# Kernel optimization log

Measured on AMD Instinct MI355X. Metric: run time of the kernel, lower is better.

The kernel has to match this reference:

```python
import jax, jax.numpy as jnp
import numpy as np

N_BINS = 256
HOP = 80


def _gru(xs, Wih, Whh, bih, bhh, reverse=False):
    """Single-layer unidirectional GRU, PyTorch gate layout (r, z, n).
    xs: (T, B, I); Wih: (3H, I); Whh: (3H, H). Returns (T, B, H)."""
    H = Whh.shape[1]
    gi = jnp.einsum('tbi,gi->tbg', xs, Wih) + bih  # precompute input projections

    def step(h, gi_t):
        gh = h @ Whh.T + bhh
        ir, iz, inn = jnp.split(gi_t, 3, axis=-1)
        hr, hz, hn = jnp.split(gh, 3, axis=-1)
        r = jax.nn.sigmoid(ir + hr)
        z = jax.nn.sigmoid(iz + hz)
        n = jnp.tanh(inn + r * hn)
        h_new = (1.0 - z) * n + z * h
        return h_new, h_new

    h0 = jnp.zeros((xs.shape[1], H), xs.dtype)
    _, ys = jax.lax.scan(step, h0, gi, reverse=reverse)
    return ys


def _quantize(w):
    # continuous [-1, 1] -> bin index in [0, N_BINS-1]
    return jnp.clip(jnp.floor((w + 1.0) * (N_BINS / 2)), 0, N_BINS - 1).astype(jnp.int32)


def _forward(x, y, p):
    # --- encode: 2-layer bidirectional GRU over mel frames ---
    c = x
    for l in ('m0', 'm1'):
        f = _gru(c, p[l + 'f_Wih'], p[l + 'f_Whh'], p[l + 'f_bih'], p[l + 'f_bhh'])
        bwd = _gru(c, p[l + 'b_Wih'], p[l + 'b_Whh'], p[l + 'b_bih'], p[l + 'b_bhh'], reverse=True)
        c = jnp.concatenate([f, bwd], axis=-1)  # (t_m, b, 2*dim_enc)
    # nearest-neighbor upsample in time (matches F.interpolate default 'nearest')
    c = jnp.repeat(c, HOP, axis=0)  # (t_w, b, 2*dim_enc)

    # --- teacher forcing: shift waveform right, vectorize via embedding ---
    b = x.shape[1]
    w = jnp.concatenate([jnp.zeros((1, b), y.dtype), y[:-1]], axis=0)
    e = p['E'][_quantize(w)]  # (t_w, b, dim_vec)

    # --- wav GRU + projection + GELU ---
    o = _gru(jnp.concatenate([e, c], axis=-1), p['w_Wih'], p['w_Whh'], p['w_bih'], p['w_bhh'])
    o = jax.nn.gelu(o @ p['Wp'].T + p['bp'], approximate=False)  # (t_w, b, dim_proj)

    # --- categorical neg log prob over quantized targets ---
    logits = o @ p['Wd'].T + p['bd']  # (t_w, b, N_BINS)
    logp = jax.nn.log_softmax(logits, axis=-1)
    tgt = _quantize(y)
    nll = -jnp.mean(jnp.take_along_axis(logp, tgt[..., None], axis=-1))
    return nll


def setup_inputs() -> dict:
    key = jax.random.key(0)
    ks = iter(jax.random.split(key, 64))

    def rn(shape, s=0.08):
        return jax.random.normal(next(ks), shape, jnp.float32) * s

    t_m, b, dm = 32, 4, 80
    de, dv, dd, dp = 128, 256, 896, 512
    d = {}
    d['x'] = jax.random.normal(next(ks), (t_m, b, dm), jnp.float32)
    d['y'] = jax.random.uniform(next(ks), (t_m * HOP, b), jnp.float32, minval=-1.0, maxval=1.0)
    for name, i in [('m0f', dm), ('m0b', dm), ('m1f', 2 * de), ('m1b', 2 * de)]:
        d[name + '_Wih'] = rn((3 * de, i))
        d[name + '_Whh'] = rn((3 * de, de))
        d[name + '_bih'] = rn((3 * de,))
        d[name + '_bhh'] = rn((3 * de,))
    d['w_Wih'] = rn((3 * dd, 2 * de + dv))
    d['w_Whh'] = rn((3 * dd, dd))
    d['w_bih'] = rn((3 * dd,))
    d['w_bhh'] = rn((3 * dd,))
    d['Wp'] = rn((dp, dd))
    d['bp'] = rn((dp,))
    d['E'] = rn((N_BINS, dv))
    d['Wd'] = rn((N_BINS, dp))
    d['bd'] = rn((N_BINS,))
    return d


def reference(x, y, m0f_Wih, m0f_Whh, m0f_bih, m0f_bhh, m0b_Wih, m0b_Whh, m0b_bih, m0b_bhh,
              m1f_Wih, m1f_Whh, m1f_bih, m1f_bhh, m1b_Wih, m1b_Whh, m1b_bih, m1b_bhh,
              w_Wih, w_Whh, w_bih, w_bhh, Wp, bp, E, Wd, bd):
    p = dict(m0f_Wih=m0f_Wih, m0f_Whh=m0f_Whh, m0f_bih=m0f_bih, m0f_bhh=m0f_bhh,
             m0b_Wih=m0b_Wih, m0b_Whh=m0b_Whh, m0b_bih=m0b_bih, m0b_bhh=m0b_bhh,
             m1f_Wih=m1f_Wih, m1f_Whh=m1f_Whh, m1f_bih=m1f_bih, m1f_bhh=m1f_bhh,
             m1b_Wih=m1b_Wih, m1b_Whh=m1b_Whh, m1b_bih=m1b_bih, m1b_bhh=m1b_bhh,
             w_Wih=w_Wih, w_Whh=w_Whh, w_bih=w_bih, w_bhh=w_bhh,
             Wp=Wp, bp=bp, E=E, Wd=Wd, bd=bd)
    return _forward(x, y, p)
```

## Files before the change

### kernel.cpp

```cpp
#include <hip/hip_runtime.h>
#include <stdint.h>
#include <math.h>

typedef __attribute__((ext_vector_type(8))) short bf16x8;
typedef __attribute__((ext_vector_type(4))) float f32x4;
typedef __attribute__((ext_vector_type(4))) unsigned int u32x4;

#define BATCH 4
#define T_M 32
#define DE 128
#define T_W 2560
#define NWG 56

__device__ __forceinline__ float b2f(unsigned short h) {
  return __uint_as_float(((unsigned int)h) << 16);
}
__device__ __forceinline__ unsigned short f2b(float f) {
  unsigned int u = __float_as_uint(f);
  u = u + 0x7fffu + ((u >> 16) & 1u);
  return (unsigned short)(u >> 16);
}
__device__ __forceinline__ float blo(unsigned int u){ return __uint_as_float(u << 16); }
__device__ __forceinline__ float bhi(unsigned int u){ return __uint_as_float(u & 0xffff0000u); }
__device__ __forceinline__ float sigm(float x){
  return __builtin_amdgcn_rcpf(1.f + __expf(-x));
}
__device__ __forceinline__ float tanh_fast(float x){
  float x2 = fminf(fmaxf(x + x, -30.f), 30.f);
  return 1.f - 2.f * __builtin_amdgcn_rcpf(__expf(x2) + 1.f);
}
__device__ __forceinline__ float gelu_exact(float x){ return 0.5f * x * (1.f + erff(x * 0.70710678118654752f)); }

__global__ __launch_bounds__(256) void k_cast(const float* __restrict__ src,
                                              unsigned short* __restrict__ dst, int n)
{
  int i = blockIdx.x * 256 + threadIdx.x;
  if (i < n) dst[i] = f2b(src[i]);
}

__global__ __launch_bounds__(256) void k_prep_whh(const float* __restrict__ whh,
                                                  unsigned short* __restrict__ out)
{
  int idx = blockIdx.x * 256 + threadIdx.x;
  if (idx >= 224 * 28 * 512) return;
  int j    = idx & 7;
  int r16  = (idx >> 3) & 15;
  int quad = (idx >> 7) & 3;
  int kc   = (idx >> 9) % 28;
  int G    = (idx >> 9) / 28;
  unsigned short val = 0;
  if (r16 < 12) {
    int row = (r16 >> 2) * 896 + G * 4 + (r16 & 3);
    int col = kc * 32 + quad * 8 + j;
    val = f2b(whh[(size_t)row * 896 + col]);
  }
  out[idx] = val;
}

__global__ __launch_bounds__(384) void k_gi_enc(
    const float* __restrict__ in, const float* __restrict__ Wih,
    const float* __restrict__ bih, float* __restrict__ out, int K)
{
  __shared__ float in_s[256];
  int tb = blockIdx.x;
  for (int i = threadIdx.x; i < K; i += 384) in_s[i] = in[tb * K + i];
  __syncthreads();
  int row = threadIdx.x;
  float acc = bih[row];
  const float* wr = Wih + row * K;
  for (int k = 0; k < K; ++k) acc += in_s[k] * wr[k];
  out[tb * 384 + row] = acc;
}

__global__ __launch_bounds__(512) void k_scan_enc(
    const float* __restrict__ gi_f, const float* __restrict__ gi_b,
    const float* __restrict__ whh_f, const float* __restrict__ bhh_f,
    const float* __restrict__ whh_b, const float* __restrict__ bhh_b,
    float* __restrict__ c_out)
{
  const int dir = blockIdx.x, tid = threadIdx.x;
  const float* gi  = dir ? gi_b  : gi_f;
  const float* whh = dir ? whh_b : whh_f;
  const float* bhh = dir ? bhh_b : bhh_f;
  __shared__ unsigned short h_s[BATCH][DE + 8];
  __shared__ float gh_s[384][4];
  __shared__ float bhh_s[384];
  for (int i = tid; i < 384; i += 512) bhh_s[i] = bhh[i];
  for (int i = tid; i < BATCH * (DE + 8); i += 512) ((unsigned short*)h_s)[i] = 0;
  __syncthreads();
  for (int s = 0; s < T_M; ++s) {
    int t = dir ? (T_M - 1 - s) : s;
    #pragma unroll
    for (int k3 = 0; k3 < 3; ++k3) {
      int d = tid + 512 * k3;
      int row = d >> 2, b = d & 3;
      const float* wr = whh + row * DE;
      float acc = 0.f;
      for (int j = 0; j < DE; j += 8) {
        float4 w0 = *(const float4*)(wr + j);
        float4 w1 = *(const float4*)(wr + j + 4);
        uint4  hv = *(const uint4*)&h_s[b][j];
        acc += w0.x * blo(hv.x) + w0.y * bhi(hv.x) + w0.z * blo(hv.y) + w0.w * bhi(hv.y);
        acc += w1.x * blo(hv.z) + w1.y * bhi(hv.z) + w1.z * blo(hv.w) + w1.w * bhi(hv.w);
      }
      gh_s[row][b] = acc + bhh_s[row];
    }
    __syncthreads();
    {
      int u = tid >> 2, b = tid & 3;
      const float* git = gi + (t * BATCH + b) * 384;
      float r = sigm(git[u] + gh_s[u][b]);
      float z = sigm(git[DE + u] + gh_s[DE + u][b]);
      float n = tanh_fast(git[2 * DE + u] + r * gh_s[2 * DE + u][b]);
      float hold = b2f(h_s[b][u]);
      float hnew = (1.f - z) * n + z * hold;
      c_out[(t * BATCH + b) * 256 + dir * DE + u] = hnew;
      h_s[b][u] = f2b(hnew);
    }
    __syncthreads();
  }
}

__global__ __launch_bounds__(256) void k_mgemm(
    const unsigned short* __restrict__ A, const unsigned short* __restrict__ B,
    const float* __restrict__ bias, void* __restrict__ C,
    int M, int N, int K, int act, int c_bf16, int swz, int afuse,
    const unsigned short* __restrict__ Eb, const unsigned short* __restrict__ c1b,
    const float* __restrict__ yw)
{
  __shared__ unsigned short As[128][40];
  __shared__ unsigned short Bs[128][40];
  const int tid = threadIdx.x;
  const int m0 = blockIdx.x * 128, n0 = blockIdx.y * 128;
  const int lane = tid & 63, wave = tid >> 6;
  const int wy = wave >> 1, wx = wave & 1;
  const int row16 = lane & 15, quad = lane >> 4;
  const int sr = tid >> 1, sc = (tid & 1) * 16;
  const unsigned short* arow0 = nullptr;
  const unsigned short* arow1 = nullptr;
  if (afuse) {
    int row = m0 + sr, tt = row >> 2, b = row & 3;
    float w = (tt == 0) ? 0.f : yw[(tt - 1) * 4 + b];
    int q = (int)floorf((w + 1.f) * 128.f);
    q = q < 0 ? 0 : (q > 255 ? 255 : q);
    arow0 = Eb + q * 256;
    arow1 = c1b + ((tt / 80) * 4 + b) * 256;
  }
  f32x4 acc[4][4] = {};
  for (int kt = 0; kt < K; kt += 32) {
    uint4 av, av2;
    if (afuse) {
      int kk = kt + sc;
      const unsigned short* src = (kk < 256) ? (arow0 + kk) : (arow1 + kk - 256);
      av  = *(const uint4*)src;
      av2 = *(const uint4*)(src + 8);
    } else {
      av  = *(const uint4*)(A + (size_t)(m0 + sr) * K + kt + sc);
      av2 = *(const uint4*)(A + (size_t)(m0 + sr) * K + kt + sc + 8);
    }
    uint4 bv  = *(const uint4*)(B + (size_t)(n0 + sr) * K + kt + sc);
    uint4 bv2 = *(const uint4*)(B + (size_t)(n0 + sr) * K + kt + sc + 8);
    __syncthreads();
    *(uint4*)&As[sr][sc] = av; *(uint4*)&As[sr][sc + 8] = av2;
    *(uint4*)&Bs[sr][sc] = bv; *(uint4*)&Bs[sr][sc + 8] = bv2;
    __syncthreads();
    bf16x8 af[4], bf[4];
    #pragma unroll
    for (int i = 0; i < 4; ++i) af[i] = *(const bf16x8*)&As[wy * 64 + i * 16 + row16][quad * 8];
    #pragma unroll
    for (int j = 0; j < 4; ++j) bf[j] = *(const bf16x8*)&Bs[wx * 64 + j * 16 + row16][quad * 8];
    #pragma unroll
    for (int i = 0; i < 4; ++i)
      #pragma unroll
      for (int j = 0; j < 4; ++j)
        acc[i][j] = __builtin_amdgcn_mfma_f32_16x16x32_bf16(af[i], bf[j], acc[i][j], 0, 0, 0);
  }
  #pragma unroll
  for (int i = 0; i < 4; ++i) {
    #pragma unroll
    for (int j = 0; j < 4; ++j) {
      int col = n0 + wx * 64 + j * 16 + row16;
      float bs = bias[col];
      #pragma unroll
      for (int r = 0; r < 4; ++r) {
        int row = m0 + wy * 64 + i * 16 + quad * 4 + r;
        float v = acc[i][j][r] + bs;
        if (act) v = gelu_exact(v);
        if (swz) {
          int t = row >> 2, b = row & 3;
          int g = col / 896, rem = col - g * 896;
          int G = rem >> 2, u = rem & 3;
          ((unsigned short*)C)[(size_t)(t * 224 + G) * 48 + g * 16 + b * 4 + u] = f2b(v);
        } else if (c_bf16) {
          ((unsigned short*)C)[(size_t)row * N + col] = f2b(v);
        } else {
          ((float*)C)[(size_t)row * N + col] = v;
        }
      }
    }
  }
}

__global__ __launch_bounds__(256, 1) void k_wav_rnn(
    const unsigned short* __restrict__ whh_p,
    const float* __restrict__ bhh,
    const unsigned short* __restrict__ gp_,
    unsigned int* __restrict__ hslots,
    unsigned int* __restrict__ O32)
{
  const int wg = blockIdx.x, tid = threadIdx.x;
  const int lane = tid & 63, wave = tid >> 6;
  const int G = wg * 4 + wave;

  __shared__ unsigned short h_lds[2][4][912];
  __shared__ float phh[4][3][4][4];

  const int r16 = lane & 15, quad = lane >> 4, bb = lane & 3;
  const int fu = (lane >> 2) & 3, fb = lane & 3;

  bf16x8 wf[28];
  {
    const bf16x8* W8 = (const bf16x8*)whh_p + (size_t)G * 28 * 64;
    #pragma unroll
    for (int kc = 0; kc < 28; ++kc)
      wf[kc] = W8[(kc * 4 + quad) * 16 + r16];
  }

  const float br_ = bhh[G * 4 + fu];
  const float bz_ = bhh[896 + G * 4 + fu];
  const float bn_ = bhh[1792 + G * 4 + fu];
  float hprev = 0.f;
  const unsigned short* gl0 = gp_ + (size_t)G * 48 + fb * 4 + fu;
  unsigned short cr = gl0[0], cz = gl0[16], cn = gl0[32];

  const int p0 = tid, p1 = tid + 256, p2 = tid + 512;
  const int p3 = (tid < 128) ? tid + 768 : tid;
  const int pb0 = p0 / 224, pG0 = p0 - pb0 * 224;
  const int pb1 = p1 / 224, pG1 = p1 - pb1 * 224;
  const int pb2 = p2 / 224, pG2 = p2 - pb2 * 224;
  const int pb3 = p3 / 224, pG3 = p3 - pb3 * 224;

  const unsigned long long base0 = (unsigned long long)hslots;
  const unsigned long long base1 = base0 + 14336ull;

  for (int t = 0; t < T_W; ++t) {
    const unsigned long long hb = (t & 1) ? base1 : base0;
    unsigned long long a0 = hb + ((unsigned long long)p0 << 4);
    unsigned long long a1 = hb + ((unsigned long long)p1 << 4);
    unsigned long long a2 = hb + ((unsigned long long)p2 << 4);
    unsigned long long a3 = hb + ((unsigned long long)p3 << 4);
    u32x4 s0, s1, s2, s3;
    const unsigned int tg = (unsigned int)t;
    for (;;) {
      asm volatile(
        "global_load_dwordx4 %0, %4, off sc0 sc1\n"
        "global_load_dwordx4 %1, %5, off sc0 sc1\n"
        "global_load_dwordx4 %2, %6, off sc0 sc1\n"
        "global_load_dwordx4 %3, %7, off sc0 sc1\n"
        "s_waitcnt vmcnt(0)"
        : "=&v"(s0), "=&v"(s1), "=&v"(s2), "=&v"(s3)
        : "v"(a0), "v"(a1), "v"(a2), "v"(a3)
        : "memory");
      unsigned int bad = (s0.z ^ tg) | (s1.z ^ tg) | (s2.z ^ tg) | (s3.z ^ tg);
      if (!__any(bad != 0)) break;
      __builtin_amdgcn_s_sleep(1);
    }

    int tn = (t + 1 < T_W) ? (t + 1) : t;
    const unsigned short* gp = gp_ + (size_t)tn * 10752 + G * 48 + fb * 4 + fu;
    unsigned short nr_ = gp[0], nz_ = gp[16], nn_ = gp[32];

    *(uint2*)&h_lds[t & 1][pb0][pG0 * 4] = make_uint2(s0.x, s0.y);
    *(uint2*)&h_lds[t & 1][pb1][pG1 * 4] = make_uint2(s1.x, s1.y);
    *(uint2*)&h_lds[t & 1][pb2][pG2 * 4] = make_uint2(s2.x, s2.y);
    *(uint2*)&h_lds[t & 1][pb3][pG3 * 4] = make_uint2(s3.x, s3.y);
    __syncthreads();

    f32x4 ac0 = {}, ac1 = {}, ac2 = {}, ac3 = {};
    #pragma unroll
    for (int kc = 0; kc < 28; kc += 4) {
      bf16x8 h0 = *(const bf16x8*)&h_lds[t & 1][bb][(kc + 0) * 32 + quad * 8];
      bf16x8 h1 = *(const bf16x8*)&h_lds[t & 1][bb][(kc + 1) * 32 + quad * 8];
      bf16x8 h2 = *(const bf16x8*)&h_lds[t & 1][bb][(kc + 2) * 32 + quad * 8];
      bf16x8 h3 = *(const bf16x8*)&h_lds[t & 1][bb][(kc + 3) * 32 + quad * 8];
      ac0 = __builtin_amdgcn_mfma_f32_16x16x32_bf16(wf[kc + 0], h0, ac0, 0, 0, 0);
      ac1 = __builtin_amdgcn_mfma_f32_16x16x32_bf16(wf[kc + 1], h1, ac1, 0, 0, 0);
      ac2 = __builtin_amdgcn_mfma_f32_16x16x32_bf16(wf[kc + 2], h2, ac2, 0, 0, 0);
      ac3 = __builtin_amdgcn_mfma_f32_16x16x32_bf16(wf[kc + 3], h3, ac3, 0, 0, 0);
    }
    f32x4 ac;
    ac[0] = ac0[0] + ac1[0] + ac2[0] + ac3[0];
    ac[1] = ac0[1] + ac1[1] + ac2[1] + ac3[1];
    ac[2] = ac0[2] + ac1[2] + ac2[2] + ac3[2];
    ac[3] = ac0[3] + ac1[3] + ac2[3] + ac3[3];

    if (r16 < 4 && quad < 3)
      *(f32x4*)&phh[wave][quad][r16][0] = ac;
    asm volatile("s_waitcnt lgkmcnt(0)" ::: "memory");

    float pr = phh[wave][0][fb][fu];
    float pz = phh[wave][1][fb][fu];
    float pn = phh[wave][2][fb][fu];
    float r = sigm(b2f(cr) + br_ + pr);
    float z = sigm(b2f(cz) + bz_ + pz);
    float n = tanh_fast(b2f(cn) + bn_ + r * pn);
    float h = (1.f - z) * n + z * hprev;
    hprev = h;
    unsigned int hu = f2b(h);
    cr = nr_; cz = nz_; cn = nn_;

    int b = lane & 3;
    unsigned int u0v = (unsigned int)__shfl((int)hu, 0 + b);
    unsigned int u1v = (unsigned int)__shfl((int)hu, 4 + b);
    unsigned int u2v = (unsigned int)__shfl((int)hu, 8 + b);
    unsigned int u3v = (unsigned int)__shfl((int)hu, 12 + b);
    if (lane < 4) {
      u32x4 pkt;
      pkt.x = (u0v & 0xffffu) | (u1v << 16);
      pkt.y = (u2v & 0xffffu) | (u3v << 16);
      pkt.z = (unsigned int)(t + 1);
      pkt.w = 0u;
      unsigned long long sa = (((t + 1) & 1) ? base1 : base0)
                            + (unsigned long long)((b * 224 + G) << 4);
      asm volatile("global_store_dwordx4 %0, %1, off sc0 sc1"
                   :: "v"(sa), "v"(pkt) : "memory");
      *(uint2*)(O32 + (size_t)(t * 4 + b) * 448 + G * 2) = make_uint2(pkt.x, pkt.y);
    }
  }
}

__global__ __launch_bounds__(256) void k_nll(
    const float* __restrict__ logits, const float* __restrict__ y,
    float* __restrict__ acc)
{
  int wid = threadIdx.x >> 6, lane = threadIdx.x & 63;
  int row = blockIdx.x * 4 + wid;
  const float* lr = logits + (size_t)row * 256;
  float v0 = lr[lane], v1 = lr[lane + 64], v2 = lr[lane + 128], v3 = lr[lane + 192];
  float mx = fmaxf(fmaxf(v0, v1), fmaxf(v2, v3));
  for (int off = 32; off > 0; off >>= 1) mx = fmaxf(mx, __shfl_xor(mx, off));
  float se = __expf(v0 - mx) + __expf(v1 - mx) + __expf(v2 - mx) + __expf(v3 - mx);
  for (int off = 32; off > 0; off >>= 1) se += __shfl_xor(se, off);
  if (lane == 0) {
    float w = y[row];
    int q = (int)floorf((w + 1.f) * 128.f);
    q = q < 0 ? 0 : (q > 255 ? 255 : q);
    float contrib = (logf(se) + mx) - lr[q];
    atomicAdd(acc, contrib);
  }
}

__global__ void k_final(const float* __restrict__ acc, float* __restrict__ out) {
  out[0] = acc[0] * (1.f / 10240.f);
}

extern "C" void kernel_launch(void* const* d_in, const int* in_sizes, int n_in,
                              void* d_out, int out_size, void* d_ws, size_t ws_size,
                              hipStream_t stream)
{
  const float* x       = (const float*)d_in[0];
  const float* y       = (const float*)d_in[1];
  const float* m0f_Wih = (const float*)d_in[2];
  const float* m0f_Whh = (const float*)d_in[3];
  const float* m0f_bih = (const float*)d_in[4];
  const float* m0f_bhh = (const float*)d_in[5];
  const float* m0b_Wih = (const float*)d_in[6];
  const float* m0b_Whh = (const float*)d_in[7];
  const float* m0b_bih = (const float*)d_in[8];
  const float* m0b_bhh = (const float*)d_in[9];
  const float* m1f_Wih = (const float*)d_in[10];
  const float* m1f_Whh = (const float*)d_in[11];
  const float* m1f_bih = (const float*)d_in[12];
  const float* m1f_bhh = (const float*)d_in[13];
  const float* m1b_Wih = (const float*)d_in[14];
  const float* m1b_Whh = (const float*)d_in[15];
  const float* m1b_bih = (const float*)d_in[16];
  const float* m1b_bhh = (const float*)d_in[17];
  const float* w_Wih   = (const float*)d_in[18];
  const float* w_Whh   = (const float*)d_in[19];
  const float* w_bih   = (const float*)d_in[20];
  const float* w_bhh   = (const float*)d_in[21];
  const float* Wp      = (const float*)d_in[22];
  const float* bp      = (const float*)d_in[23];
  const float* E       = (const float*)d_in[24];
  const float* Wd      = (const float*)d_in[25];
  const float* bd      = (const float*)d_in[26];

  char* ws = (char*)d_ws;
  size_t off = 0;
  auto alloc = [&](size_t bytes) -> void* {
    void* p = ws + off;
    off += (bytes + 255) & ~(size_t)255;
    return p;
  };
  float*        nacc   = (float*)alloc(64);
  unsigned int* hslots = (unsigned int*)alloc(2 * 896 * 16);
  size_t misc_bytes = off;

  float* c0   = (float*)alloc((size_t)32 * 4 * 256 * 4);
  float* c1   = (float*)alloc((size_t)32 * 4 * 256 * 4);
  float* gi0f = (float*)alloc((size_t)32 * 4 * 384 * 4);
  float* gi0b = (float*)alloc((size_t)32 * 4 * 384 * 4);
  float* gi1f = (float*)alloc((size_t)32 * 4 * 384 * 4);
  float* gi1b = (float*)alloc((size_t)32 * 4 * 384 * 4);
  unsigned short* Eb    = (unsigned short*)alloc((size_t)256 * 256 * 2);
  unsigned short* c1b   = (unsigned short*)alloc((size_t)32 * 4 * 256 * 2);
  unsigned short* gpack = (unsigned short*)alloc((size_t)2560 * 224 * 48 * 2);
  unsigned int*   O32   = (unsigned int*)alloc((size_t)10240 * 448 * 4);
  unsigned short* O2    = (unsigned short*)alloc((size_t)10240 * 512 * 2);
  float*          LG    = (float*)alloc((size_t)10240 * 256 * 4);
  unsigned short* Wih_b = (unsigned short*)alloc((size_t)2688 * 512 * 2);
  unsigned short* Whh_p = (unsigned short*)alloc((size_t)224 * 28 * 512 * 2);
  unsigned short* Wp_b  = (unsigned short*)alloc((size_t)512 * 896 * 2);
  unsigned short* Wd_b  = (unsigned short*)alloc((size_t)256 * 512 * 2);

  hipMemsetAsync(d_ws, 0, misc_bytes, stream);

  k_cast<<<(2688 * 512 + 255) / 256, 256, 0, stream>>>(w_Wih, Wih_b, 2688 * 512);
  k_cast<<<(512 * 896 + 255) / 256, 256, 0, stream>>>(Wp, Wp_b, 512 * 896);
  k_cast<<<(256 * 512 + 255) / 256, 256, 0, stream>>>(Wd, Wd_b, 256 * 512);
  k_cast<<<(256 * 256 + 255) / 256, 256, 0, stream>>>(E, Eb, 256 * 256);
  k_prep_whh<<<(224 * 28 * 512 + 255) / 256, 256, 0, stream>>>(w_Whh, Whh_p);

  k_gi_enc<<<128, 384, 0, stream>>>(x, m0f_Wih, m0f_bih, gi0f, 80);
  k_gi_enc<<<128, 384, 0, stream>>>(x, m0b_Wih, m0b_bih, gi0b, 80);
  k_scan_enc<<<2, 512, 0, stream>>>(gi0f, gi0b, m0f_Whh, m0f_bhh, m0b_Whh, m0b_bhh, c0);
  k_gi_enc<<<128, 384, 0, stream>>>(c0, m1f_Wih, m1f_bih, gi1f, 256);
  k_gi_enc<<<128, 384, 0, stream>>>(c0, m1b_Wih, m1b_bih, gi1b, 256);
  k_scan_enc<<<2, 512, 0, stream>>>(gi1f, gi1b, m1f_Whh, m1f_bhh, m1b_Whh, m1b_bhh, c1);
  k_cast<<<(32 * 4 * 256 + 255) / 256, 256, 0, stream>>>(c1, c1b, 32 * 4 * 256);

  k_mgemm<<<dim3(80, 21), 256, 0, stream>>>(nullptr, Wih_b, w_bih, (void*)gpack,
                                            10240, 2688, 512, 0, 1, 1, 1, Eb, c1b, y);

  k_wav_rnn<<<NWG, 256, 0, stream>>>(Whh_p, w_bhh, gpack, hslots, O32);

  k_mgemm<<<dim3(80, 4), 256, 0, stream>>>((const unsigned short*)O32, Wp_b, bp,
                                           (void*)O2, 10240, 512, 896, 1, 1, 0, 0,
                                           nullptr, nullptr, nullptr);
  k_mgemm<<<dim3(80, 2), 256, 0, stream>>>(O2, Wd_b, bd, (void*)LG,
                                           10240, 256, 512, 0, 0, 0, 0,
                                           nullptr, nullptr, nullptr);
  k_nll<<<2560, 256, 0, stream>>>(LG, y, nacc);
  k_final<<<1, 1, 0, stream>>>(nacc, (float*)d_out);
}
```

Before: 6.020 ms.

## Merge prep casts, fuse c1 cast into scan, drop spin sleep, tree-reduce NLL

Merges the four weight-cast kernels and the Whh pack kernel into one launch, and has the second encoder scan write the bf16 copy of its output so the separate cast launch goes away. The gi_enc dot product is vectorised with float4 loads. The s_sleep in the wav-RNN spin-wait is removed to cut polling latency on the serial recurrence, at the cost of heavier memory polling. The NLL atomic accumulation is replaced by per-block partials plus a 256-thread reduction, which also makes the sum order deterministic.

```diff
diff --git a/kernel.cpp b/kernel.cpp
--- a/kernel.cpp
+++ b/kernel.cpp
@@ -31,17 +31,24 @@
 }
 __device__ __forceinline__ float gelu_exact(float x){ return 0.5f * x * (1.f + erff(x * 0.70710678118654752f)); }
 
-__global__ __launch_bounds__(256) void k_cast(const float* __restrict__ src,
-                                              unsigned short* __restrict__ dst, int n)
-{
-  int i = blockIdx.x * 256 + threadIdx.x;
-  if (i < n) dst[i] = f2b(src[i]);
-}
-
-__global__ __launch_bounds__(256) void k_prep_whh(const float* __restrict__ whh,
-                                                  unsigned short* __restrict__ out)
+__global__ __launch_bounds__(256) void k_prep(
+    const float* __restrict__ wih, const float* __restrict__ wp,
+    const float* __restrict__ wd, const float* __restrict__ e,
+    const float* __restrict__ whh,
+    unsigned short* __restrict__ wih_b, unsigned short* __restrict__ wp_b,
+    unsigned short* __restrict__ wd_b, unsigned short* __restrict__ eb,
+    unsigned short* __restrict__ whh_p)
 {
   int idx = blockIdx.x * 256 + threadIdx.x;
+  const int N0 = 2688 * 512, N1 = 512 * 896, N2 = 256 * 512, N3 = 256 * 256;
+  if (idx < N0) { wih_b[idx] = f2b(wih[idx]); return; }
+  idx -= N0;
+  if (idx < N1) { wp_b[idx] = f2b(wp[idx]); return; }
+  idx -= N1;
+  if (idx < N2) { wd_b[idx] = f2b(wd[idx]); return; }
+  idx -= N2;
+  if (idx < N3) { eb[idx] = f2b(e[idx]); return; }
+  idx -= N3;
   if (idx >= 224 * 28 * 512) return;
   int j    = idx & 7;
   int r16  = (idx >> 3) & 15;
@@ -54,7 +61,7 @@
     int col = kc * 32 + quad * 8 + j;
     val = f2b(whh[(size_t)row * 896 + col]);
   }
-  out[idx] = val;
+  whh_p[idx] = val;
 }
 
 __global__ __launch_bounds__(384) void k_gi_enc(
@@ -68,7 +75,11 @@
   int row = threadIdx.x;
   float acc = bih[row];
   const float* wr = Wih + row * K;
-  for (int k = 0; k < K; ++k) acc += in_s[k] * wr[k];
+  for (int k = 0; k < K; k += 4) {
+    float4 w = *(const float4*)(wr + k);
+    float4 v = *(const float4*)(in_s + k);
+    acc += w.x * v.x + w.y * v.y + w.z * v.z + w.w * v.w;
+  }
   out[tb * 384 + row] = acc;
 }
 
@@ -76,7 +87,7 @@
     const float* __restrict__ gi_f, const float* __restrict__ gi_b,
     const float* __restrict__ whh_f, const float* __restrict__ bhh_f,
     const float* __restrict__ whh_b, const float* __restrict__ bhh_b,
-    float* __restrict__ c_out)
+    float* __restrict__ c_out, unsigned short* __restrict__ cb)
 {
   const int dir = blockIdx.x, tid = threadIdx.x;
   const float* gi  = dir ? gi_b  : gi_f;
@@ -114,7 +125,9 @@
       float n = tanh_fast(git[2 * DE + u] + r * gh_s[2 * DE + u][b]);
       float hold = b2f(h_s[b][u]);
       float hnew = (1.f - z) * n + z * hold;
-      c_out[(t * BATCH + b) * 256 + dir * DE + u] = hnew;
+      int oi = (t * BATCH + b) * 256 + dir * DE + u;
+      c_out[oi] = hnew;
+      if (cb) cb[oi] = f2b(hnew);
       h_s[b][u] = f2b(hnew);
     }
     __syncthreads();
@@ -263,7 +276,6 @@
         : "memory");
       unsigned int bad = (s0.z ^ tg) | (s1.z ^ tg) | (s2.z ^ tg) | (s3.z ^ tg);
       if (!__any(bad != 0)) break;
-      __builtin_amdgcn_s_sleep(1);
     }
 
     int tn = (t + 1 < T_W) ? (t + 1) : t;
@@ -331,8 +343,9 @@
 
 __global__ __launch_bounds__(256) void k_nll(
     const float* __restrict__ logits, const float* __restrict__ y,
-    float* __restrict__ acc)
-{
+    float* __restrict__ partials)
+{
+  __shared__ float ps[4];
   int wid = threadIdx.x >> 6, lane = threadIdx.x & 63;
   int row = blockIdx.x * 4 + wid;
   const float* lr = logits + (size_t)row * 256;
@@ -345,13 +358,23 @@
     float w = y[row];
     int q = (int)floorf((w + 1.f) * 128.f);
     q = q < 0 ? 0 : (q > 255 ? 255 : q);
-    float contrib = (logf(se) + mx) - lr[q];
-    atomicAdd(acc, contrib);
-  }
-}
-
-__global__ void k_final(const float* __restrict__ acc, float* __restrict__ out) {
-  out[0] = acc[0] * (1.f / 10240.f);
+    ps[wid] = (logf(se) + mx) - lr[q];
+  }
+  __syncthreads();
+  if (threadIdx.x == 0) partials[blockIdx.x] = ps[0] + ps[1] + ps[2] + ps[3];
+}
+
+__global__ __launch_bounds__(256) void k_final(const float* __restrict__ partials,
+                                               float* __restrict__ out)
+{
+  __shared__ float s[4];
+  int tid = threadIdx.x;
+  float a = 0.f;
+  for (int i = tid; i < 2560; i += 256) a += partials[i];
+  for (int off = 32; off > 0; off >>= 1) a += __shfl_xor(a, off);
+  if ((tid & 63) == 0) s[tid >> 6] = a;
+  __syncthreads();
+  if (tid == 0) out[0] = (s[0] + s[1] + s[2] + s[3]) * (1.f / 10240.f);
 }
 
 extern "C" void kernel_launch(void* const* d_in, const int* in_sizes, int n_in,
@@ -393,7 +416,6 @@
     off += (bytes + 255) & ~(size_t)255;
     return p;
   };
-  float*        nacc   = (float*)alloc(64);
   unsigned int* hslots = (unsigned int*)alloc(2 * 896 * 16);
   size_t misc_bytes = off;
 
@@ -409,6 +431,7 @@
   unsigned int*   O32   = (unsigned int*)alloc((size_t)10240 * 448 * 4);
   unsigned short* O2    = (unsigned short*)alloc((size_t)10240 * 512 * 2);
   float*          LG    = (float*)alloc((size_t)10240 * 256 * 4);
+  float*          PT    = (float*)alloc((size_t)2560 * 4);
   unsigned short* Wih_b = (unsigned short*)alloc((size_t)2688 * 512 * 2);
   unsigned short* Whh_p = (unsigned short*)alloc((size_t)224 * 28 * 512 * 2);
   unsigned short* Wp_b  = (unsigned short*)alloc((size_t)512 * 896 * 2);
@@ -416,19 +439,20 @@
 
   hipMemsetAsync(d_ws, 0, misc_bytes, stream);
 
-  k_cast<<<(2688 * 512 + 255) / 256, 256, 0, stream>>>(w_Wih, Wih_b, 2688 * 512);
-  k_cast<<<(512 * 896 + 255) / 256, 256, 0, stream>>>(Wp, Wp_b, 512 * 896);
-  k_cast<<<(256 * 512 + 255) / 256, 256, 0, stream>>>(Wd, Wd_b, 256 * 512);
-  k_cast<<<(256 * 256 + 255) / 256, 256, 0, stream>>>(E, Eb, 256 * 256);
-  k_prep_whh<<<(224 * 28 * 512 + 255) / 256, 256, 0, stream>>>(w_Whh, Whh_p);
+  {
+    int total = 2688 * 512 + 512 * 896 + 256 * 512 + 256 * 256 + 224 * 28 * 512;
+    k_prep<<<(total + 255) / 256, 256, 0, stream>>>(
+        w_Wih, Wp, Wd, E, w_Whh, Wih_b, Wp_b, Wd_b, Eb, Whh_p);
+  }
 
   k_gi_enc<<<128, 384, 0, stream>>>(x, m0f_Wih, m0f_bih, gi0f, 80);
   k_gi_enc<<<128, 384, 0, stream>>>(x, m0b_Wih, m0b_bih, gi0b, 80);
-  k_scan_enc<<<2, 512, 0, stream>>>(gi0f, gi0b, m0f_Whh, m0f_bhh, m0b_Whh, m0b_bhh, c0);
+  k_scan_enc<<<2, 512, 0, stream>>>(gi0f, gi0b, m0f_Whh, m0f_bhh, m0b_Whh, m0b_bhh,
+                                    c0, nullptr);
   k_gi_enc<<<128, 384, 0, stream>>>(c0, m1f_Wih, m1f_bih, gi1f, 256);
   k_gi_enc<<<128, 384, 0, stream>>>(c0, m1b_Wih, m1b_bih, gi1b, 256);
-  k_scan_enc<<<2, 512, 0, stream>>>(gi1f, gi1b, m1f_Whh, m1f_bhh, m1b_Whh, m1b_bhh, c1);
-  k_cast<<<(32 * 4 * 256 + 255) / 256, 256, 0, stream>>>(c1, c1b, 32 * 4 * 256);
+  k_scan_enc<<<2, 512, 0, stream>>>(gi1f, gi1b, m1f_Whh, m1f_bhh, m1b_Whh, m1b_bhh,
+                                    c1, c1b);
 
   k_mgemm<<<dim3(80, 21), 256, 0, stream>>>(nullptr, Wih_b, w_bih, (void*)gpack,
                                             10240, 2688, 512, 0, 1, 1, 1, Eb, c1b, y);
@@ -441,6 +465,6 @@
   k_mgemm<<<dim3(80, 2), 256, 0, stream>>>(O2, Wd_b, bd, (void*)LG,
                                            10240, 256, 512, 0, 0, 0, 0,
                                            nullptr, nullptr, nullptr);
-  k_nll<<<2560, 256, 0, stream>>>(LG, y, nacc);
-  k_final<<<1, 1, 0, stream>>>(nacc, (float*)d_out);
-}
+  k_nll<<<2560, 256, 0, stream>>>(LG, y, PT);
+  k_final<<<1, 256, 0, stream>>>(PT, (float*)d_out);
+}
```

Result: faster. 5.765 ms (-4.2%).
